# Optimization experiments

Measured on AMD Instinct MI355X. Metric: run time of the kernel, lower is better.

Reference implementation:

```python
import jax, jax.numpy as jnp
import numpy as np

K_SIZE = 3      # kernel height/width
STRIDE = 1
SPARSITY = 0.7  # fraction of zero weights in the kernel


def setup_inputs() -> dict:
    key = jax.random.key(0)
    k1, k2, k3 = jax.random.split(key, 3)
    N, C, H, W = 32, 128, 56, 56
    F = 256
    Kdim = C * K_SIZE * K_SIZE  # 1152
    inputs = jax.random.normal(k1, (N, C, H, W), dtype=jnp.float32)
    limit = np.sqrt(6.0 / (F + Kdim)).astype(np.float32)
    vals = jax.random.uniform(k2, (F, Kdim), dtype=jnp.float32, minval=-limit, maxval=limit)
    mask = (jax.random.uniform(k3, (F, Kdim)) >= SPARSITY).astype(jnp.float32)
    kernel = vals * mask
    return {"inputs": inputs, "kernel": kernel}


def reference(inputs, kernel):
    k, s = K_SIZE, STRIDE
    # Original: transpose NCHW -> (N, W, H, C), extract_patches over (W, H)
    x = jnp.transpose(inputs, (0, 3, 2, 1))  # (N, W, H, C)
    N, Wd, Hd, C = x.shape
    Wo = (Wd - k) // s + 1
    Ho = (Hd - k) // s + 1
    # im2col: patch flatten order = [w_offset, h_offset, channel], matching tf.image.extract_patches
    patches = jnp.stack(
        [x[:, i : i + (Wo - 1) * s + 1 : s, j : j + (Ho - 1) * s + 1 : s, :]
         for i in range(k) for j in range(k)],
        axis=3,
    )  # (N, Wo, Ho, k*k, C)
    flat = patches.reshape(N, Wo, Ho, k * k * C)
    # CSR spmm == dense matmul with the (structurally sparse) dense kernel
    out = jnp.einsum('nwhk,fk->nfwh', flat, kernel)  # (N, F, Wo, Ho)
    return out
```

## Files before the change

### kernel.cpp

```cpp
#include <hip/hip_runtime.h>

typedef _Float16 half8 __attribute__((ext_vector_type(8)));
typedef float f32x16 __attribute__((ext_vector_type(16)));
typedef float f32x4 __attribute__((ext_vector_type(4)));

#define N_IMG 32
#define C_IN  128
#define H_IN  56
#define W_IN  56
#define F_OUT 256
#define HO    54
#define WO    54
#define KKDIM 1152
#define NKB   18

#define T2_BYTES (N_IMG * W_IN * H_IN * C_IN * 2)
#define BP_OFF   T2_BYTES
#define BP_BYTES (NKB * F_OUT * 64 * 2)
#define WS_NEED  (BP_OFF + BP_BYTES)

#define SLAB_I_STRIDE 14336
#define A_BYTES  (6 * SLAB_I_STRIDE)
#define B_CHUNK  32768
#define SMEM_BYTES (A_BYTES + 2 * B_CHUNK)

__global__ __launch_bounds__(256) void k_transpose(const float* __restrict__ in,
                                                   _Float16* __restrict__ t2) {
    __shared__ _Float16 Lt[128 * 57];
    const int n  = blockIdx.y;
    const int hh = blockIdx.x;
    const int t  = threadIdx.x;

    {
        const int ww = t & 63;
        const int c0 = t >> 6;
        if (ww < 56) {
            for (int c = c0; c < 128; c += 4)
                Lt[c * 57 + ww] = (_Float16)in[(((size_t)(n * 128 + c) * 56) + hh) * 56 + ww];
        }
    }
    __syncthreads();

    {
        const int ci  = t & 15;
        const int wwi = t >> 4;
        const int X   = (hh & 15) << 4;
        for (int ww = wwi; ww < 56; ww += 16) {
            union { _Float16 h[8]; int4 v; } u;
#pragma unroll
            for (int jj = 0; jj < 8; ++jj)
                u.h[jj] = Lt[(ci * 8 + jj) * 57 + ww];
            char* dst = (char*)t2 + ((size_t)((n * 56 + ww) * 56 + hh)) * 256 + ((ci * 16) ^ X);
            *(int4*)dst = u.v;
        }
    }
}

__global__ __launch_bounds__(256) void k_weights(const float* __restrict__ kern,
                                                 _Float16* __restrict__ bp) {
    const int tid = blockIdx.x * 256 + threadIdx.x;
    if (tid >= F_OUT * KKDIM) return;
    const int f = tid / KKDIM;
    const int k = tid % KKDIM;
    const int kb = k >> 6, kin = k & 63;
    const _Float16 v = (_Float16)kern[tid];
    char* dst = (char*)bp + kb * B_CHUNK + f * 128 + ((kin * 2) ^ ((f & 7) << 4));
    *(_Float16*)dst = v;
}

typedef const __attribute__((address_space(1))) unsigned int guint;
typedef __attribute__((address_space(3))) unsigned int luint;

__global__ __launch_bounds__(512, 2) void k_gemm(const _Float16* __restrict__ t2,
                                                 const _Float16* __restrict__ bp,
                                                 float* __restrict__ out) {
    extern __shared__ char smem[];
    char* As  = smem;
    char* Bs0 = smem + A_BYTES;
    char* Bs1 = smem + A_BYTES + B_CHUNK;

    const int tid  = threadIdx.x;
    const int lane = tid & 63;
    const int wid  = tid >> 6;
    const int wm   = wid >> 1;
    const int wf   = wid & 1;
    const int ln31 = lane & 31;
    const int kin2 = (lane >> 5) * 16;
    const int n  = blockIdx.y;
    const int w0 = blockIdx.x * 4;

    int navail = 56 - w0; if (navail > 6) navail = 6;
    const int bytesA = navail * SLAB_I_STRIDE;
    const char* t2n = (const char*)t2 + (size_t)(n * 56 + w0) * 56 * 256;
    for (int o = tid * 16; o < bytesA; o += 8192)
        __builtin_amdgcn_global_load_lds((guint*)(t2n + o), (luint*)(As + o), 16, 0, 0);

    const char* bpc = (const char*)bp;
    for (int o = tid * 16; o < B_CHUNK; o += 8192)
        __builtin_amdgcn_global_load_lds((guint*)(bpc + o), (luint*)(Bs0 + o), 16, 0, 0);

    f32x16 acc[2][4];
#pragma unroll
    for (int m2 = 0; m2 < 2; ++m2)
#pragma unroll
        for (int ft = 0; ft < 4; ++ft)
#pragma unroll
            for (int e = 0; e < 16; ++e)
                acc[m2][ft][e] = 0.0f;

    __syncthreads();

    for (int kb = 0; kb < NKB; ++kb) {
        char* curB = (kb & 1) ? Bs1 : Bs0;
        if (kb < NKB - 1) {
            char* nxtB = (kb & 1) ? Bs0 : Bs1;
            const char* src = bpc + (kb + 1) * B_CHUNK;
#pragma unroll
            for (int oi = 0; oi < 4; ++oi) {
                int o = tid * 16 + oi * 8192;
                __builtin_amdgcn_global_load_lds((guint*)(src + o), (luint*)(nxtB + o), 16, 0, 0);
            }
        }

        const int ij  = kb >> 1;
        const int iq  = ij / 3;
        const int jq  = ij - iq * 3;
        const int ch2 = (kb & 1) * 128;
        const int iwb = (wm + iq) * SLAB_I_STRIDE;
        const int hh0 = ln31 + jq;
        const int Xa  = (hh0 & 15) << 4;
        const int Xb  = (ln31 & 7) << 4;

#pragma unroll
        for (int s = 0; s < 4; ++s) {
            const int cb = ch2 + s * 32 + kin2;
            half8 aF[2];
#pragma unroll
            for (int m2 = 0; m2 < 2; ++m2) {
                const int hh = hh0 + m2 * 32;
                aF[m2] = *(const half8*)(As + iwb + hh * 256 + (cb ^ Xa));
            }
            half8 bF[4];
#pragma unroll
            for (int ft = 0; ft < 4; ++ft) {
                const int f = wf * 128 + ft * 32 + ln31;
                bF[ft] = *(const half8*)(curB + f * 128 + ((s * 32 + kin2) ^ Xb));
            }
#pragma unroll
            for (int m2 = 0; m2 < 2; ++m2)
#pragma unroll
                for (int ft = 0; ft < 4; ++ft)
                    acc[m2][ft] = __builtin_amdgcn_mfma_f32_32x32x16_f16(aF[m2], bF[ft], acc[m2][ft], 0, 0, 0);
        }
        __syncthreads();
    }

    const int w = w0 + wm;
    if (w < WO) {
        const int hi4 = (lane >> 5) * 4;
#pragma unroll
        for (int m2 = 0; m2 < 2; ++m2) {
#pragma unroll
            for (int ft = 0; ft < 4; ++ft) {
                const int f = wf * 128 + ft * 32 + ln31;
                float* op = out + ((size_t)(n * 256 + f) * 54 + w) * 54;
#pragma unroll
                for (int q = 0; q < 4; ++q) {
                    const int hb = m2 * 32 + q * 8 + hi4;
                    if (hb + 3 < HO) {
                        f32x4 v = { acc[m2][ft][4 * q + 0], acc[m2][ft][4 * q + 1],
                                    acc[m2][ft][4 * q + 2], acc[m2][ft][4 * q + 3] };
                        *(f32x4*)(op + hb) = v;
                    } else if (hb < HO) {
                        op[hb]     = acc[m2][ft][4 * q + 0];
                        op[hb + 1] = acc[m2][ft][4 * q + 1];
                    }
                }
            }
        }
    }
}

__global__ __launch_bounds__(256) void k_naive(const float* __restrict__ in,
                                               const float* __restrict__ kern,
                                               float* __restrict__ out) {
    const int idx = blockIdx.x * 256 + threadIdx.x;
    const int total = N_IMG * F_OUT * WO * HO;
    if (idx >= total) return;
    const int h = idx % 54;
    const int w = (idx / 54) % 54;
    const int f = (idx / (54 * 54)) % 256;
    const int n = idx / (54 * 54 * 256);
    float s = 0.f;
    for (int ij = 0; ij < 9; ++ij) {
        const int i = ij / 3, j = ij % 3;
        const float* ip = in + ((size_t)(n * 128) * 56 + (h + j)) * 56 + (w + i);
        const float* kp = kern + (size_t)f * KKDIM + ij * 128;
        for (int c = 0; c < 128; ++c) s += ip[(size_t)c * 3136] * kp[c];
    }
    out[idx] = s;
}

extern "C" void kernel_launch(void* const* d_in, const int* in_sizes, int n_in,
                              void* d_out, int out_size, void* d_ws, size_t ws_size,
                              hipStream_t stream) {
    const float* in   = (const float*)d_in[0];
    const float* kern = (const float*)d_in[1];
    float* out = (float*)d_out;

    if (ws_size < (size_t)WS_NEED) {
        const int total = N_IMG * F_OUT * WO * HO;
        k_naive<<<(total + 255) / 256, 256, 0, stream>>>(in, kern, out);
        return;
    }

    _Float16* t2 = (_Float16*)d_ws;
    _Float16* bp = (_Float16*)((char*)d_ws + BP_OFF);

    k_transpose<<<dim3(56, 32), 256, 0, stream>>>(in, t2);
    k_weights<<<(F_OUT * KKDIM + 255) / 256, 256, 0, stream>>>(kern, bp);

    (void)hipFuncSetAttribute((const void*)k_gemm,
                              hipFuncAttributeMaxDynamicSharedMemorySize, SMEM_BYTES);
    k_gemm<<<dim3(14, 32), 512, SMEM_BYTES, stream>>>(t2, bp, out);
}
```

Before: 217.6 us.

## Double GEMM block to 16 waves, split H across waves, add explicit waitcnt barriers

The GEMM workgroup grows from 512 to 1024 threads. Each wave now owns one 32-row H half, a single A fragment and 4 accumulator tiles instead of 2x4, which halves accumulator registers and doubles the waves available to hide latency. The B double-buffer pipeline drops __syncthreads in favour of manual s_waitcnt vmcnt plus raw s_barrier, and MFMA issue is wrapped in s_setprio. The A region is padded so out-of-slab row reads stay inside the A buffer. In exchange, each B fragment is reused less, so LDS read traffic rises. The aggressive launch bounds (1024, 4) may also over-constrain register allocation.

```diff
diff --git a/kernel.cpp b/kernel.cpp
--- a/kernel.cpp
+++ b/kernel.cpp
@@ -20,9 +20,12 @@
 #define WS_NEED  (BP_OFF + BP_BYTES)
 
 #define SLAB_I_STRIDE 14336
-#define A_BYTES  (6 * SLAB_I_STRIDE)
-#define B_CHUNK  32768
-#define SMEM_BYTES (A_BYTES + 2 * B_CHUNK)
+#define A_BYTES   (6 * SLAB_I_STRIDE)
+#define A_REGION  88576
+#define B_CHUNK   32768
+#define SMEM_BYTES (A_REGION + 2 * B_CHUNK)
+
+#define ASM_BAR() asm volatile("s_barrier" ::: "memory")
 
 __global__ __launch_bounds__(256) void k_transpose(const float* __restrict__ in,
                                                    _Float16* __restrict__ t2) {
@@ -71,18 +74,19 @@
 typedef const __attribute__((address_space(1))) unsigned int guint;
 typedef __attribute__((address_space(3))) unsigned int luint;
 
-__global__ __launch_bounds__(512, 2) void k_gemm(const _Float16* __restrict__ t2,
-                                                 const _Float16* __restrict__ bp,
-                                                 float* __restrict__ out) {
+__global__ __launch_bounds__(1024, 4) void k_gemm(const _Float16* __restrict__ t2,
+                                                  const _Float16* __restrict__ bp,
+                                                  float* __restrict__ out) {
     extern __shared__ char smem[];
     char* As  = smem;
-    char* Bs0 = smem + A_BYTES;
-    char* Bs1 = smem + A_BYTES + B_CHUNK;
+    char* Bs0 = smem + A_REGION;
+    char* Bs1 = smem + A_REGION + B_CHUNK;
 
     const int tid  = threadIdx.x;
     const int lane = tid & 63;
     const int wid  = tid >> 6;
-    const int wm   = wid >> 1;
+    const int wm   = wid >> 2;
+    const int wh   = (wid >> 1) & 1;
     const int wf   = wid & 1;
     const int ln31 = lane & 31;
     const int kin2 = (lane >> 5) * 16;
@@ -92,89 +96,78 @@
     int navail = 56 - w0; if (navail > 6) navail = 6;
     const int bytesA = navail * SLAB_I_STRIDE;
     const char* t2n = (const char*)t2 + (size_t)(n * 56 + w0) * 56 * 256;
-    for (int o = tid * 16; o < bytesA; o += 8192)
+    for (int o = tid * 16; o < bytesA; o += 16384)
         __builtin_amdgcn_global_load_lds((guint*)(t2n + o), (luint*)(As + o), 16, 0, 0);
 
     const char* bpc = (const char*)bp;
-    for (int o = tid * 16; o < B_CHUNK; o += 8192)
-        __builtin_amdgcn_global_load_lds((guint*)(bpc + o), (luint*)(Bs0 + o), 16, 0, 0);
-
-    f32x16 acc[2][4];
-#pragma unroll
-    for (int m2 = 0; m2 < 2; ++m2)
-#pragma unroll
-        for (int ft = 0; ft < 4; ++ft)
-#pragma unroll
-            for (int e = 0; e < 16; ++e)
-                acc[m2][ft][e] = 0.0f;
-
-    __syncthreads();
+    __builtin_amdgcn_global_load_lds((guint*)(bpc + tid * 16), (luint*)(Bs0 + tid * 16), 16, 0, 0);
+    __builtin_amdgcn_global_load_lds((guint*)(bpc + tid * 16 + 16384), (luint*)(Bs0 + tid * 16 + 16384), 16, 0, 0);
+
+    f32x16 acc[4];
+#pragma unroll
+    for (int ft = 0; ft < 4; ++ft)
+#pragma unroll
+        for (int e = 0; e < 16; ++e)
+            acc[ft][e] = 0.0f;
+
+    const int Xb = (ln31 & 7) << 4;
+    const int fb128 = (wf * 128 + ln31) * 128;
 
     for (int kb = 0; kb < NKB; ++kb) {
-        char* curB = (kb & 1) ? Bs1 : Bs0;
+        const char* curB = (kb & 1) ? Bs1 : Bs0;
         if (kb < NKB - 1) {
             char* nxtB = (kb & 1) ? Bs0 : Bs1;
             const char* src = bpc + (kb + 1) * B_CHUNK;
-#pragma unroll
-            for (int oi = 0; oi < 4; ++oi) {
-                int o = tid * 16 + oi * 8192;
-                __builtin_amdgcn_global_load_lds((guint*)(src + o), (luint*)(nxtB + o), 16, 0, 0);
-            }
-        }
+            __builtin_amdgcn_global_load_lds((guint*)(src + tid * 16), (luint*)(nxtB + tid * 16), 16, 0, 0);
+            __builtin_amdgcn_global_load_lds((guint*)(src + tid * 16 + 16384), (luint*)(nxtB + tid * 16 + 16384), 16, 0, 0);
+            asm volatile("s_waitcnt vmcnt(2)" ::: "memory");
+        } else {
+            asm volatile("s_waitcnt vmcnt(0)" ::: "memory");
+        }
+        ASM_BAR();
 
         const int ij  = kb >> 1;
         const int iq  = ij / 3;
         const int jq  = ij - iq * 3;
         const int ch2 = (kb & 1) * 128;
-        const int iwb = (wm + iq) * SLAB_I_STRIDE;
-        const int hh0 = ln31 + jq;
-        const int Xa  = (hh0 & 15) << 4;
-        const int Xb  = (ln31 & 7) << 4;
+        const int hh  = wh * 32 + ln31 + jq;
+        const int Xa  = (hh & 15) << 4;
+        const int abase = (wm + iq) * SLAB_I_STRIDE + hh * 256;
 
 #pragma unroll
         for (int s = 0; s < 4; ++s) {
             const int cb = ch2 + s * 32 + kin2;
-            half8 aF[2];
-#pragma unroll
-            for (int m2 = 0; m2 < 2; ++m2) {
-                const int hh = hh0 + m2 * 32;
-                aF[m2] = *(const half8*)(As + iwb + hh * 256 + (cb ^ Xa));
-            }
+            half8 aF = *(const half8*)(As + abase + (cb ^ Xa));
             half8 bF[4];
 #pragma unroll
-            for (int ft = 0; ft < 4; ++ft) {
-                const int f = wf * 128 + ft * 32 + ln31;
-                bF[ft] = *(const half8*)(curB + f * 128 + ((s * 32 + kin2) ^ Xb));
-            }
-#pragma unroll
-            for (int m2 = 0; m2 < 2; ++m2)
-#pragma unroll
-                for (int ft = 0; ft < 4; ++ft)
-                    acc[m2][ft] = __builtin_amdgcn_mfma_f32_32x32x16_f16(aF[m2], bF[ft], acc[m2][ft], 0, 0, 0);
-        }
-        __syncthreads();
+            for (int ft = 0; ft < 4; ++ft)
+                bF[ft] = *(const half8*)(curB + fb128 + ft * 32 * 128 + ((s * 32 + kin2) ^ Xb));
+            __builtin_amdgcn_s_setprio(1);
+#pragma unroll
+            for (int ft = 0; ft < 4; ++ft)
+                acc[ft] = __builtin_amdgcn_mfma_f32_32x32x16_f16(aF, bF[ft], acc[ft], 0, 0, 0);
+            __builtin_amdgcn_s_setprio(0);
+        }
+        ASM_BAR();
     }
 
     const int w = w0 + wm;
     if (w < WO) {
         const int hi4 = (lane >> 5) * 4;
 #pragma unroll
-        for (int m2 = 0; m2 < 2; ++m2) {
-#pragma unroll
-            for (int ft = 0; ft < 4; ++ft) {
-                const int f = wf * 128 + ft * 32 + ln31;
-                float* op = out + ((size_t)(n * 256 + f) * 54 + w) * 54;
-#pragma unroll
-                for (int q = 0; q < 4; ++q) {
-                    const int hb = m2 * 32 + q * 8 + hi4;
-                    if (hb + 3 < HO) {
-                        f32x4 v = { acc[m2][ft][4 * q + 0], acc[m2][ft][4 * q + 1],
-                                    acc[m2][ft][4 * q + 2], acc[m2][ft][4 * q + 3] };
-                        *(f32x4*)(op + hb) = v;
-                    } else if (hb < HO) {
-                        op[hb]     = acc[m2][ft][4 * q + 0];
-                        op[hb + 1] = acc[m2][ft][4 * q + 1];
-                    }
+        for (int ft = 0; ft < 4; ++ft) {
+            const int f = wf * 128 + ft * 32 + ln31;
+            float* op = out + ((size_t)(n * 256 + f) * 54 + w) * 54;
+#pragma unroll
+            for (int q = 0; q < 4; ++q) {
+                const int hb = wh * 32 + q * 8 + hi4;
+                if (hb + 3 < HO) {
+                    f32x4 v = { acc[ft][4 * q + 0], acc[ft][4 * q + 1],
+                                acc[ft][4 * q + 2], acc[ft][4 * q + 3] };
+                    *(f32x4*)(op + hb) = v;
+                } else if (hb < HO) {
+                    op[hb]     = acc[ft][4 * q + 0];
+                    op[hb + 1] = acc[ft][4 * q + 1];
                 }
             }
         }
@@ -222,5 +215,5 @@
 
     (void)hipFuncSetAttribute((const void*)k_gemm,
                               hipFuncAttributeMaxDynamicSharedMemorySize, SMEM_BYTES);
-    k_gemm<<<dim3(14, 32), 512, SMEM_BYTES, stream>>>(t2, bp, out);
-}
+    k_gemm<<<dim3(14, 32), 1024, SMEM_BYTES, stream>>>(t2, bp, out);
+}
```

After: 215.6 us. Within noise of the previous version (-0.9%).

## Interleave B-chunk prefetch across k-substeps with explicit barriers and MFMA priority

Applied to the files above, without the earlier changes.

Restructures the GEMM main loop so the next weight chunk's global-to-LDS loads are spread across the four k-substeps rather than issued together at the top. Each substep gets explicit s_barrier and waitcnt pairs, a sched_barrier, and raises wave priority around the MFMA block. The A region is padded slightly and address arithmetic is hoisted. This aims to overlap memory traffic with MFMA issue in a ping-pong style, at the cost of more barriers per iteration and reliance on hand-placed waitcnt correctness.

```diff
diff --git a/kernel.cpp b/kernel.cpp
--- a/kernel.cpp
+++ b/kernel.cpp
@@ -20,9 +20,12 @@
 #define WS_NEED  (BP_OFF + BP_BYTES)
 
 #define SLAB_I_STRIDE 14336
-#define A_BYTES  (6 * SLAB_I_STRIDE)
-#define B_CHUNK  32768
-#define SMEM_BYTES (A_BYTES + 2 * B_CHUNK)
+#define A_BYTES   (6 * SLAB_I_STRIDE)
+#define A_REGION  88576
+#define B_CHUNK   32768
+#define SMEM_BYTES (A_REGION + 2 * B_CHUNK)
+
+#define ASM_BAR() asm volatile("s_barrier" ::: "memory")
 
 __global__ __launch_bounds__(256) void k_transpose(const float* __restrict__ in,
                                                    _Float16* __restrict__ t2) {
@@ -76,8 +79,8 @@
                                                  float* __restrict__ out) {
     extern __shared__ char smem[];
     char* As  = smem;
-    char* Bs0 = smem + A_BYTES;
-    char* Bs1 = smem + A_BYTES + B_CHUNK;
+    char* Bs0 = smem + A_REGION;
+    char* Bs1 = smem + A_REGION + B_CHUNK;
 
     const int tid  = threadIdx.x;
     const int lane = tid & 63;
@@ -96,8 +99,10 @@
         __builtin_amdgcn_global_load_lds((guint*)(t2n + o), (luint*)(As + o), 16, 0, 0);
 
     const char* bpc = (const char*)bp;
-    for (int o = tid * 16; o < B_CHUNK; o += 8192)
-        __builtin_amdgcn_global_load_lds((guint*)(bpc + o), (luint*)(Bs0 + o), 16, 0, 0);
+#pragma unroll
+    for (int q = 0; q < 4; ++q)
+        __builtin_amdgcn_global_load_lds((guint*)(bpc + tid * 16 + q * 8192),
+                                         (luint*)(Bs0 + tid * 16 + q * 8192), 16, 0, 0);
 
     f32x16 acc[2][4];
 #pragma unroll
@@ -108,51 +113,66 @@
             for (int e = 0; e < 16; ++e)
                 acc[m2][ft][e] = 0.0f;
 
-    __syncthreads();
+    asm volatile("s_waitcnt vmcnt(0)" ::: "memory");
+    ASM_BAR();
+
+    const int Xb = (ln31 & 7) << 4;
+    const int fb128 = (wf * 128 + ln31) * 128;
 
     for (int kb = 0; kb < NKB; ++kb) {
-        char* curB = (kb & 1) ? Bs1 : Bs0;
-        if (kb < NKB - 1) {
-            char* nxtB = (kb & 1) ? Bs0 : Bs1;
-            const char* src = bpc + (kb + 1) * B_CHUNK;
-#pragma unroll
-            for (int oi = 0; oi < 4; ++oi) {
-                int o = tid * 16 + oi * 8192;
-                __builtin_amdgcn_global_load_lds((guint*)(src + o), (luint*)(nxtB + o), 16, 0, 0);
-            }
-        }
+        const char* curB = (kb & 1) ? Bs1 : Bs0;
+        char* nxtB = (kb & 1) ? Bs0 : Bs1;
+        const char* src = bpc + (kb + 1) * B_CHUNK;
 
         const int ij  = kb >> 1;
         const int iq  = ij / 3;
         const int jq  = ij - iq * 3;
         const int ch2 = (kb & 1) * 128;
-        const int iwb = (wm + iq) * SLAB_I_STRIDE;
         const int hh0 = ln31 + jq;
         const int Xa  = (hh0 & 15) << 4;
-        const int Xb  = (ln31 & 7) << 4;
+        const int abase = (wm + iq) * SLAB_I_STRIDE + hh0 * 256;
 
 #pragma unroll
         for (int s = 0; s < 4; ++s) {
             const int cb = ch2 + s * 32 + kin2;
-            half8 aF[2];
-#pragma unroll
-            for (int m2 = 0; m2 < 2; ++m2) {
-                const int hh = hh0 + m2 * 32;
-                aF[m2] = *(const half8*)(As + iwb + hh * 256 + (cb ^ Xa));
+            half8 aF0 = *(const half8*)(As + abase + (cb ^ Xa));
+            half8 aF1 = *(const half8*)(As + abase + 32 * 256 + (cb ^ Xa));
+            half8 bF[4];
+#pragma unroll
+            for (int ft = 0; ft < 4; ++ft)
+                bF[ft] = *(const half8*)(curB + fb128 + ft * 4096 + ((s * 32 + kin2) ^ Xb));
+
+            if (kb < NKB - 1) {
+                if (s == 0) {
+                    __builtin_amdgcn_global_load_lds((guint*)(src + tid * 16),
+                                                     (luint*)(nxtB + tid * 16), 16, 0, 0);
+                    __builtin_amdgcn_global_load_lds((guint*)(src + tid * 16 + 8192),
+                                                     (luint*)(nxtB + tid * 16 + 8192), 16, 0, 0);
+                } else if (s == 1) {
+                    __builtin_amdgcn_global_load_lds((guint*)(src + tid * 16 + 16384),
+                                                     (luint*)(nxtB + tid * 16 + 16384), 16, 0, 0);
+                } else if (s == 2) {
+                    __builtin_amdgcn_global_load_lds((guint*)(src + tid * 16 + 24576),
+                                                     (luint*)(nxtB + tid * 16 + 24576), 16, 0, 0);
+                }
             }
-            half8 bF[4];
+
+            ASM_BAR();
+            asm volatile("s_waitcnt lgkmcnt(0)" ::: "memory");
+            __builtin_amdgcn_sched_barrier(0);
+
+            __builtin_amdgcn_s_setprio(1);
 #pragma unroll
             for (int ft = 0; ft < 4; ++ft) {
-                const int f = wf * 128 + ft * 32 + ln31;
-                bF[ft] = *(const half8*)(curB + f * 128 + ((s * 32 + kin2) ^ Xb));
+                acc[0][ft] = __builtin_amdgcn_mfma_f32_32x32x16_f16(aF0, bF[ft], acc[0][ft], 0, 0, 0);
+                acc[1][ft] = __builtin_amdgcn_mfma_f32_32x32x16_f16(aF1, bF[ft], acc[1][ft], 0, 0, 0);
             }
-#pragma unroll
-            for (int m2 = 0; m2 < 2; ++m2)
-#pragma unroll
-                for (int ft = 0; ft < 4; ++ft)
-                    acc[m2][ft] = __builtin_amdgcn_mfma_f32_32x32x16_f16(aF[m2], bF[ft], acc[m2][ft], 0, 0, 0);
-        }
-        __syncthreads();
+            __builtin_amdgcn_s_setprio(0);
+
+            if (s == 3)
+                asm volatile("s_waitcnt vmcnt(0)" ::: "memory");
+            ASM_BAR();
+        }
     }
 
     const int w = w0 + wm;
```

Measured after the change: 225.2 us. +3.5%, slower.
